# Optimization experiments

Measured on AMD Instinct MI355X. Metric: run time of the kernel, lower is better.

The kernel has to match this reference:

```python
import jax, jax.numpy as jnp
import numpy as np

B, N, D, H, KD, VD, O = 64, 2048, 256, 8, 32, 32, 256
LARGE = 1e9
EPS = 1e-10


def setup_inputs() -> dict:
    key = jax.random.key(0)
    ks = jax.random.split(key, 8)
    return {
        "q_data": jax.random.normal(ks[0], (B, N, D), dtype=jnp.float32),
        "m_data": jax.random.normal(ks[1], (B, N, D), dtype=jnp.float32),
        "q_mask": jnp.ones((B, N, 1), dtype=jnp.float32),
        "query_w": jax.random.normal(ks[2], (D, H, KD), dtype=jnp.float32) * 0.05,
        "key_w": jax.random.normal(ks[3], (D, KD), dtype=jnp.float32) * 0.05,
        "value_w": jax.random.normal(ks[4], (D, VD), dtype=jnp.float32) * 0.05,
        "gating_w": jax.random.normal(ks[5], (D, H, VD), dtype=jnp.float32) * 0.05,
        "gating_b": jnp.ones((H, VD), dtype=jnp.float32),
        "output_w": jax.random.normal(ks[6], (H, VD, O), dtype=jnp.float32) * 0.05,
        "output_b": jnp.zeros((O,), dtype=jnp.float32),
    }


def reference(q_data, m_data, q_mask, query_w, key_w, value_w, gating_w, gating_b, output_w, output_b):
    key_dim = query_w.shape[-1]
    # values/keys are shared across heads: [B, N, KD/VD]
    v = jnp.einsum('bka,ac->bkc', m_data, value_w)
    # masked mean over the query axis -> single query per batch element
    q_avg = jnp.sum(q_mask * q_data, axis=1) / (jnp.sum(q_mask, axis=1) + EPS)  # [B, D]
    q = jnp.einsum('ba,ahc->bhc', q_avg, query_w) * (key_dim ** -0.5)  # [B, H, KD]
    k = jnp.einsum('bka,ac->bkc', m_data, key_w)  # [B, N, KD]
    bias = LARGE * (q_mask[:, None, :, 0] - 1.0)  # [B, 1, N]
    logits = jnp.einsum('bhc,bkc->bhk', q, k) + bias  # [B, H, N]
    weights = jax.nn.softmax(logits, axis=-1)
    weighted_avg = jnp.einsum('bhk,bkc->bhc', weights, v)  # [B, H, VD]
    gate = jax.nn.sigmoid(jnp.einsum('bqc,chv->bqhv', q_data, gating_w) + gating_b)  # [B, N, H, VD]
    gated = weighted_avg[:, None] * gate  # broadcast single attn result over queries
    return jnp.einsum('bqhc,hco->bqo', gated, output_w) + output_b  # [B, N, O]
```

## Files before the change

kernel.cpp:

```cpp
#include <hip/hip_runtime.h>

#define B_ 64
#define N_ 2048
#define D_ 256
#define H_ 8
#define LARGE_ 1e9f
#define EPS_ 1e-10f

typedef __attribute__((ext_vector_type(4))) float f32x4;
typedef __attribute__((ext_vector_type(8))) short s16x8;

#define WS_QKBF 0
#define WS_WGP  524288
#define WS_QPART 655360
#define WS_MPART 1179648
#define WS_MX   1181696
#define WS_SM   1247232
#define WS_WA   1312768
#define WS_WMP  1378304
#define WS_WPP  1378304

__device__ __forceinline__ unsigned short f2bf(float f) {
  union { float f; unsigned u; } v; v.f = f;
  unsigned r = v.u + 0x7fffu + ((v.u >> 16) & 1u);
  return (unsigned short)(r >> 16);
}
__device__ __forceinline__ float bf2f(unsigned short s) {
  union { unsigned u; float f; } v; v.u = ((unsigned)s) << 16;
  return v.f;
}

__global__ void kA(const float* __restrict__ q_data, const float* __restrict__ q_mask,
                   const float* __restrict__ gating_w, float* __restrict__ qpart,
                   float* __restrict__ mpart, unsigned short* __restrict__ wgp) {
  int blk = blockIdx.x, t = threadIdx.x;
  if (blk < 512) {
    int b = blk >> 3, n0 = (blk & 7) * 256;
    __shared__ float msk[256];
    __shared__ float qred[4][256];
    __shared__ float mred[4];
    msk[t] = q_mask[b * N_ + n0 + t];
    __syncthreads();
    int w = t >> 6, d4 = t & 63;
    const float* qbase = q_data + ((size_t)(b * N_ + n0)) * D_;
    f32x4 acc = {0.f, 0.f, 0.f, 0.f};
    #pragma unroll 4
    for (int i = 0; i < 64; ++i) {
      int r = i * 4 + w;
      f32x4 v = *(const f32x4*)(qbase + (size_t)r * D_ + d4 * 4);
      float mk = msk[r];
      acc += v * mk;
    }
    *(f32x4*)(&qred[w][d4 * 4]) = acc;
    float mv = msk[t];
    for (int off = 32; off; off >>= 1) mv += __shfl_xor(mv, off);
    if ((t & 63) == 0) mred[t >> 6] = mv;
    __syncthreads();
    qpart[((size_t)blk) * 256 + t] = qred[0][t] + qred[1][t] + qred[2][t] + qred[3][t];
    if (t == 0) mpart[blk] = mred[0] + mred[1] + mred[2] + mred[3];
  } else {
    int base = (blk - 512) * 1024;
    for (int i = 0; i < 4; ++i) {
      int a = base + i * 256 + t;
      int sc = a >> 9, l = (a >> 3) & 63, j = a & 7;
      int s = sc >> 4, c = sc & 15, lh = l >> 4, ll = l & 15;
      int k = s * 32 + lh * 8 + j, n = c * 16 + ll;
      wgp[a] = f2bf(gating_w[k * 256 + n]);
    }
  }
}

__global__ void kB(const float* __restrict__ qpart, const float* __restrict__ mpart,
                   const float* __restrict__ query_w, const float* __restrict__ key_w,
                   unsigned short* __restrict__ qkbf) {
  int b = blockIdx.x, t = threadIdx.x;
  __shared__ float qa[256];
  __shared__ float ql[256];
  float s = 0.f;
  #pragma unroll
  for (int p = 0; p < 8; ++p) s += qpart[((size_t)(b * 8 + p)) * 256 + t];
  float ms = 0.f;
  #pragma unroll
  for (int p = 0; p < 8; ++p) ms += mpart[b * 8 + p];
  qa[t] = s / (ms + EPS_);
  __syncthreads();
  float acc = 0.f;
  #pragma unroll 4
  for (int a = 0; a < 256; ++a) acc += qa[a] * query_w[a * 256 + t];
  ql[t] = acc * 0.17677669529663687f;
  __syncthreads();
  float v8[8];
  #pragma unroll
  for (int h = 0; h < 8; ++h) {
    float v = 0.f;
    #pragma unroll
    for (int c = 0; c < 32; ++c) v += key_w[t * 32 + c] * ql[h * 32 + c];
    v8[h] = v;
  }
  int si = t >> 5, lh = (t >> 3) & 3, j = t & 7;
  unsigned short* base = qkbf + ((size_t)(b * 8 + si) * 64) * 8;
  #pragma unroll
  for (int h = 0; h < 8; ++h) {
    base[(lh * 16 + h) * 8 + j] = f2bf(v8[h]);
    base[(lh * 16 + 8 + h) * 8 + j] = 0;
  }
}

__global__ void kM(const float* __restrict__ m_data, const float* __restrict__ q_mask,
                   const unsigned short* __restrict__ qkbf, unsigned short* __restrict__ wm_part,
                   float* __restrict__ mx_part, float* __restrict__ sm_part) {
  int b = blockIdx.y, ch = blockIdx.x, n0 = ch * 64, t = threadIdx.x;
  __shared__ __align__(16) unsigned char sM[64 * 528];
  __shared__ f32x4 pW[64][2];
  __shared__ float red[4][8];
  __shared__ float hval[8];
  {
    int w = t >> 6, d4 = t & 63;
    #pragma unroll
    for (int i = 0; i < 16; ++i) {
      int r = i * 4 + w;
      f32x4 v = *(const f32x4*)(m_data + ((size_t)(b * N_ + n0 + r)) * D_ + d4 * 4);
      uint2 pp;
      pp.x = f2bf(v[0]) | ((unsigned)f2bf(v[1]) << 16);
      pp.y = f2bf(v[2]) | ((unsigned)f2bf(v[3]) << 16);
      *(uint2*)(sM + r * 528 + d4 * 8) = pp;
    }
  }
  __syncthreads();
  int lane = t & 63, w = t >> 6;
  int l15 = lane & 15, lhi = lane >> 4;
  const s16x8* A = (const s16x8*)qkbf + (size_t)b * 512;
  s16x8 areg[8];
  #pragma unroll
  for (int s = 0; s < 8; ++s) areg[s] = A[s * 64 + lane];
  f32x4 acc = {0.f, 0.f, 0.f, 0.f};
  int nrow = w * 16 + l15;
  #pragma unroll
  for (int s = 0; s < 8; ++s) {
    s16x8 bfr = *(const s16x8*)(sM + nrow * 528 + s * 64 + lhi * 16);
    acc = __builtin_amdgcn_mfma_f32_16x16x32_bf16(areg[s], bfr, acc, 0, 0, 0);
  }
  float bias = LARGE_ * (q_mask[b * N_ + n0 + nrow] - 1.f);
  float lg[4];
  #pragma unroll
  for (int r = 0; r < 4; ++r) lg[r] = (lhi < 2) ? (acc[r] + bias) : -3.4e38f;
  #pragma unroll
  for (int off = 8; off; off >>= 1)
    #pragma unroll
    for (int r = 0; r < 4; ++r) lg[r] = fmaxf(lg[r], __shfl_xor(lg[r], off));
  if (l15 == 0 && lhi < 2)
    #pragma unroll
    for (int r = 0; r < 4; ++r) red[w][lhi * 4 + r] = lg[r];
  __syncthreads();
  if (t < 8) {
    float m = fmaxf(fmaxf(red[0][t], red[1][t]), fmaxf(red[2][t], red[3][t]));
    hval[t] = m;
    mx_part[((size_t)(b * 32 + ch)) * 8 + t] = m;
  }
  __syncthreads();
  float pv[4], ps[4];
  #pragma unroll
  for (int r = 0; r < 4; ++r) {
    float M = hval[(lhi & 1) * 4 + r];
    float e = __expf(acc[r] + bias - M);
    pv[r] = e;
    ps[r] = (lhi < 2) ? e : 0.f;
  }
  if (lhi < 2) {
    f32x4 pq = {pv[0], pv[1], pv[2], pv[3]};
    pW[nrow][lhi] = pq;
  }
  #pragma unroll
  for (int off = 8; off; off >>= 1)
    #pragma unroll
    for (int r = 0; r < 4; ++r) ps[r] += __shfl_xor(ps[r], off);
  if (l15 == 0 && lhi < 2)
    #pragma unroll
    for (int r = 0; r < 4; ++r) red[w][lhi * 4 + r] = ps[r];
  __syncthreads();
  if (t < 8)
    sm_part[((size_t)(b * 32 + ch)) * 8 + t] = red[0][t] + red[1][t] + red[2][t] + red[3][t];
  f32x4 vacc[8];
  #pragma unroll
  for (int h = 0; h < 8; ++h) vacc[h] = (f32x4){0.f, 0.f, 0.f, 0.f};
  #pragma unroll 4
  for (int i = 0; i < 16; ++i) {
    int r = w * 16 + i;
    uint2 pp = *(const uint2*)(sM + r * 528 + lane * 8);
    f32x4 mv;
    mv[0] = bf2f(pp.x & 0xffff); mv[1] = bf2f(pp.x >> 16);
    mv[2] = bf2f(pp.y & 0xffff); mv[3] = bf2f(pp.y >> 16);
    f32x4 w0 = pW[r][0], w1 = pW[r][1];
    vacc[0] += mv * w0[0]; vacc[1] += mv * w0[1]; vacc[2] += mv * w0[2]; vacc[3] += mv * w0[3];
    vacc[4] += mv * w1[0]; vacc[5] += mv * w1[1]; vacc[6] += mv * w1[2]; vacc[7] += mv * w1[3];
  }
  __syncthreads();
  float* red2 = (float*)sM;
  #pragma unroll
  for (int h = 0; h < 8; ++h) *(f32x4*)(&red2[(w * 8 + h) * 256 + lane * 4]) = vacc[h];
  __syncthreads();
  float s8[8];
  #pragma unroll
  for (int h = 0; h < 8; ++h)
    s8[h] = red2[h * 256 + t] + red2[(8 + h) * 256 + t] + red2[(16 + h) * 256 + t] +
            red2[(24 + h) * 256 + t];
  uint4 u;
  u.x = f2bf(s8[0]) | ((unsigned)f2bf(s8[1]) << 16);
  u.y = f2bf(s8[2]) | ((unsigned)f2bf(s8[3]) << 16);
  u.z = f2bf(s8[4]) | ((unsigned)f2bf(s8[5]) << 16);
  u.w = f2bf(s8[6]) | ((unsigned)f2bf(s8[7]) << 16);
  *(uint4*)(wm_part + ((size_t)((b * 32 + ch) * 256 + t)) * 8) = u;
}

__global__ void kF1(const unsigned short* __restrict__ wm_part, const float* __restrict__ mx_part,
                    const float* __restrict__ sm_part, const float* __restrict__ value_w,
                    float* __restrict__ wa_g) {
  int b = blockIdx.x, t = threadIdx.x;
  __shared__ float s_mx[256], s_sm[256], scl[256];
  __shared__ float gmx[8], gden[8];
  __shared__ float wml[8][256];
  s_mx[t] = mx_part[(size_t)b * 256 + t];
  s_sm[t] = sm_part[(size_t)b * 256 + t];
  __syncthreads();
  if (t < 8) {
    float m = -3.4e38f;
    for (int c = 0; c < 32; ++c) m = fmaxf(m, s_mx[c * 8 + t]);
    gmx[t] = m;
  }
  __syncthreads();
  scl[t] = __expf(s_mx[t] - gmx[t & 7]);
  __syncthreads();
  if (t < 8) {
    float d = 0.f;
    for (int c = 0; c < 32; ++c) d += s_sm[c * 8 + t] * scl[c * 8 + t];
    gden[t] = d;
  }
  float acc[8] = {0.f, 0.f, 0.f, 0.f, 0.f, 0.f, 0.f, 0.f};
  for (int c = 0; c < 32; ++c) {
    uint4 u = *(const uint4*)(wm_part + ((size_t)((b * 32 + c) * 256 + t)) * 8);
    const float* sc = &scl[c * 8];
    acc[0] += bf2f(u.x & 0xffff) * sc[0]; acc[1] += bf2f(u.x >> 16) * sc[1];
    acc[2] += bf2f(u.y & 0xffff) * sc[2]; acc[3] += bf2f(u.y >> 16) * sc[3];
    acc[4] += bf2f(u.z & 0xffff) * sc[4]; acc[5] += bf2f(u.z >> 16) * sc[5];
    acc[6] += bf2f(u.w & 0xffff) * sc[6]; acc[7] += bf2f(u.w >> 16) * sc[7];
  }
  #pragma unroll
  for (int h = 0; h < 8; ++h) wml[h][t] = acc[h];
  __syncthreads();
  int h = t >> 5, v = t & 31;
  float s = 0.f;
  #pragma unroll 4
  for (int d = 0; d < 256; ++d) s += wml[h][d] * value_w[d * 32 + v];
  wa_g[b * 256 + t] = s / gden[h];
}

__global__ void kF2(const float* __restrict__ wa_g, const float* __restrict__ output_w,
                    unsigned short* __restrict__ wpp) {
  int blk = blockIdx.x, t = threadIdx.x;
  int b = blk >> 2, quad = blk & 3;
  __shared__ float wa[256];
  wa[t] = wa_g[b * 256 + t];
  __syncthreads();
  unsigned short* wp = wpp + (size_t)b * 65536;
  int base = quad * 16384;
  for (int it = 0; it < 64; ++it) {
    int a = base + it * 256 + t;
    int sc = a >> 9, l = (a >> 3) & 63, j = a & 7;
    int s = sc >> 4, c = sc & 15, lh = l >> 4, ll = l & 15;
    int hv = s * 32 + lh * 8 + j, o = c * 16 + ll;
    wp[a] = f2bf(wa[hv] * output_w[hv * 256 + o]);
  }
}

__global__ void __launch_bounds__(256, 4) kG(
    const float* __restrict__ q_data, const float* __restrict__ gating_b,
    const float* __restrict__ output_b, const unsigned short* __restrict__ wgp,
    const unsigned short* __restrict__ wpp, float* __restrict__ out) {
  int b = blockIdx.y, row0 = blockIdx.x * 64, t = threadIdx.x;
  __shared__ __align__(16) unsigned char sG[64 * 528];
  {
    int w = t >> 6, d4 = t & 63;
    #pragma unroll
    for (int i = 0; i < 16; ++i) {
      int r = i * 4 + w;
      f32x4 v = *(const f32x4*)(q_data + ((size_t)(b * N_ + row0 + r)) * D_ + d4 * 4);
      uint2 pp;
      pp.x = f2bf(v[0]) | ((unsigned)f2bf(v[1]) << 16);
      pp.y = f2bf(v[2]) | ((unsigned)f2bf(v[3]) << 16);
      *(uint2*)(sG + r * 528 + d4 * 8) = pp;
    }
  }
  __syncthreads();
  int lane = t & 63, cg = t >> 6;
  int l15 = lane & 15, lhi = lane >> 4;
  const f32x4 z = {0.f, 0.f, 0.f, 0.f};
  f32x4 acc[16];
  #pragma unroll
  for (int f = 0; f < 16; ++f) acc[f] = z;
  const s16x8* Bg = (const s16x8*)wgp;
  #pragma unroll
  for (int s = 0; s < 8; ++s) {
    s16x8 af[4], bfr[4];
    #pragma unroll
    for (int rt = 0; rt < 4; ++rt)
      af[rt] = *(const s16x8*)(sG + (rt * 16 + l15) * 528 + s * 64 + lhi * 16);
    #pragma unroll
    for (int ct = 0; ct < 4; ++ct) bfr[ct] = Bg[(s * 16 + cg * 4 + ct) * 64 + lane];
    #pragma unroll
    for (int rt = 0; rt < 4; ++rt)
      #pragma unroll
      for (int ct = 0; ct < 4; ++ct)
        acc[rt * 4 + ct] =
            __builtin_amdgcn_mfma_f32_16x16x32_bf16(af[rt], bfr[ct], acc[rt * 4 + ct], 0, 0, 0);
  }
  __syncthreads();
  {
    float gb[4];
    #pragma unroll
    for (int ct = 0; ct < 4; ++ct) gb[ct] = gating_b[cg * 64 + ct * 16 + l15];
    #pragma unroll
    for (int rt = 0; rt < 4; ++rt)
      #pragma unroll
      for (int ct = 0; ct < 4; ++ct) {
        int col = cg * 64 + ct * 16 + l15;
        #pragma unroll
        for (int r = 0; r < 4; ++r) {
          float x = acc[rt * 4 + ct][r] + gb[ct];
          float g = 1.f / (1.f + __expf(-x));
          int row = rt * 16 + lhi * 4 + r;
          *(unsigned short*)(sG + row * 528 + col * 2) = f2bf(g);
        }
      }
  }
  __syncthreads();
  #pragma unroll
  for (int f = 0; f < 16; ++f) acc[f] = z;
  const s16x8* Bp = (const s16x8*)wpp + (size_t)b * 8192;
  #pragma unroll
  for (int s = 0; s < 8; ++s) {
    s16x8 af[4], bfr[4];
    #pragma unroll
    for (int rt = 0; rt < 4; ++rt)
      af[rt] = *(const s16x8*)(sG + (rt * 16 + l15) * 528 + s * 64 + lhi * 16);
    #pragma unroll
    for (int ct = 0; ct < 4; ++ct) bfr[ct] = Bp[(s * 16 + cg * 4 + ct) * 64 + lane];
    #pragma unroll
    for (int rt = 0; rt < 4; ++rt)
      #pragma unroll
      for (int ct = 0; ct < 4; ++ct)
        acc[rt * 4 + ct] =
            __builtin_amdgcn_mfma_f32_16x16x32_bf16(af[rt], bfr[ct], acc[rt * 4 + ct], 0, 0, 0);
  }
  __syncthreads();
  float* fOut = (float*)sG;
  float ob[4];
  #pragma unroll
  for (int ct = 0; ct < 4; ++ct) ob[ct] = output_b[cg * 64 + ct * 16 + l15];
  #pragma unroll
  for (int p = 0; p < 2; ++p) {
    #pragma unroll
    for (int rt2 = 0; rt2 < 2; ++rt2) {
      int rt = p * 2 + rt2;
      #pragma unroll
      for (int ct = 0; ct < 4; ++ct) {
        int col = cg * 64 + ct * 16 + l15;
        #pragma unroll
        for (int r = 0; r < 4; ++r)
          fOut[(rt2 * 16 + lhi * 4 + r) * 260 + col] = acc[rt * 4 + ct][r] + ob[ct];
      }
    }
    __syncthreads();
    {
      int w = t >> 6, c4 = t & 63;
      #pragma unroll
      for (int j = 0; j < 8; ++j) {
        int r32 = j * 4 + w;
        f32x4 v = *(const f32x4*)(fOut + r32 * 260 + c4 * 4);
        *(f32x4*)(out + ((size_t)(b * N_ + row0 + p * 32 + r32)) * D_ + c4 * 4) = v;
      }
    }
    __syncthreads();
  }
}

extern "C" void kernel_launch(void* const* d_in, const int* in_sizes, int n_in,
                              void* d_out, int out_size, void* d_ws, size_t ws_size,
                              hipStream_t stream) {
  const float* q_data   = (const float*)d_in[0];
  const float* m_data   = (const float*)d_in[1];
  const float* q_mask   = (const float*)d_in[2];
  const float* query_w  = (const float*)d_in[3];
  const float* key_w    = (const float*)d_in[4];
  const float* value_w  = (const float*)d_in[5];
  const float* gating_w = (const float*)d_in[6];
  const float* gating_b = (const float*)d_in[7];
  const float* output_w = (const float*)d_in[8];
  const float* output_b = (const float*)d_in[9];
  float* out = (float*)d_out;
  char* ws = (char*)d_ws;

  unsigned short* qkbf = (unsigned short*)(ws + WS_QKBF);
  unsigned short* wgp  = (unsigned short*)(ws + WS_WGP);
  float* qpart = (float*)(ws + WS_QPART);
  float* mpart = (float*)(ws + WS_MPART);
  float* mx    = (float*)(ws + WS_MX);
  float* sm    = (float*)(ws + WS_SM);
  float* wa    = (float*)(ws + WS_WA);
  unsigned short* wmp = (unsigned short*)(ws + WS_WMP);
  unsigned short* wpp = (unsigned short*)(ws + WS_WPP);

  kA<<<576, 256, 0, stream>>>(q_data, q_mask, gating_w, qpart, mpart, wgp);
  kB<<<64, 256, 0, stream>>>(qpart, mpart, query_w, key_w, qkbf);
  kM<<<dim3(32, 64), 256, 0, stream>>>(m_data, q_mask, qkbf, wmp, mx, sm);
  kF1<<<64, 256, 0, stream>>>(wmp, mx, sm, value_w, wa);
  kF2<<<256, 256, 0, stream>>>(wa, output_w, wpp);
  kG<<<dim3(32, 64), 256, 0, stream>>>(q_data, gating_b, output_b, wgp, wpp, out);
}
```

Measured before the change: 478.4 us.

## Halve kG row tile for more blocks and stage output_w through LDS in kF2

The main gated-output kernel kG now handles 32 rows per block instead of 64. That doubles the grid, halves the accumulators and LDS per block, and raises the launch-bounds occupancy hint from 4 to 6. kF2 now copies output_w rows into shared memory with coalesced vector loads before doing the scattered, permuted bf16 packing, so it no longer makes strided global reads. The smaller kG tiles mean each weight fragment is reused across fewer rows, so wgp/wpp loads per output row roughly double.

```diff
diff --git a/kernel.cpp b/kernel.cpp
--- a/kernel.cpp
+++ b/kernel.cpp
@@ -258,30 +258,43 @@
                     unsigned short* __restrict__ wpp) {
   int blk = blockIdx.x, t = threadIdx.x;
   int b = blk >> 2, quad = blk & 3;
+  __shared__ float sOW[32 * 260];
   __shared__ float wa[256];
   wa[t] = wa_g[b * 256 + t];
-  __syncthreads();
   unsigned short* wp = wpp + (size_t)b * 65536;
-  int base = quad * 16384;
-  for (int it = 0; it < 64; ++it) {
-    int a = base + it * 256 + t;
-    int sc = a >> 9, l = (a >> 3) & 63, j = a & 7;
-    int s = sc >> 4, c = sc & 15, lh = l >> 4, ll = l & 15;
-    int hv = s * 32 + lh * 8 + j, o = c * 16 + ll;
-    wp[a] = f2bf(wa[hv] * output_w[hv * 256 + o]);
-  }
-}
-
-__global__ void __launch_bounds__(256, 4) kG(
+  for (int half = 0; half < 2; ++half) {
+    int srow = quad * 64 + half * 32;
+    __syncthreads();
+    const f32x4* src = (const f32x4*)(output_w + srow * 256);
+    #pragma unroll
+    for (int i = 0; i < 8; ++i) {
+      int idx4 = i * 256 + t;
+      f32x4 v = src[idx4];
+      int rr = idx4 >> 6, c4 = idx4 & 63;
+      *(f32x4*)(&sOW[rr * 260 + c4 * 4]) = v;
+    }
+    __syncthreads();
+    int abase = quad * 16384 + half * 8192;
+    for (int it = 0; it < 32; ++it) {
+      int a = abase + it * 256 + t;
+      int sc = a >> 9, l = (a >> 3) & 63, j = a & 7;
+      int c = sc & 15, lh = l >> 4, ll = l & 15;
+      int hvl = lh * 8 + j, o = c * 16 + ll;
+      wp[a] = f2bf(wa[srow + hvl] * sOW[hvl * 260 + o]);
+    }
+  }
+}
+
+__global__ void __launch_bounds__(256, 6) kG(
     const float* __restrict__ q_data, const float* __restrict__ gating_b,
     const float* __restrict__ output_b, const unsigned short* __restrict__ wgp,
     const unsigned short* __restrict__ wpp, float* __restrict__ out) {
-  int b = blockIdx.y, row0 = blockIdx.x * 64, t = threadIdx.x;
-  __shared__ __align__(16) unsigned char sG[64 * 528];
+  int b = blockIdx.y, row0 = blockIdx.x * 32, t = threadIdx.x;
+  __shared__ __align__(16) unsigned char sG[32 * 528];
   {
     int w = t >> 6, d4 = t & 63;
     #pragma unroll
-    for (int i = 0; i < 16; ++i) {
+    for (int i = 0; i < 8; ++i) {
       int r = i * 4 + w;
       f32x4 v = *(const f32x4*)(q_data + ((size_t)(b * N_ + row0 + r)) * D_ + d4 * 4);
       uint2 pp;
@@ -294,20 +307,20 @@
   int lane = t & 63, cg = t >> 6;
   int l15 = lane & 15, lhi = lane >> 4;
   const f32x4 z = {0.f, 0.f, 0.f, 0.f};
-  f32x4 acc[16];
-  #pragma unroll
-  for (int f = 0; f < 16; ++f) acc[f] = z;
+  f32x4 acc[8];
+  #pragma unroll
+  for (int f = 0; f < 8; ++f) acc[f] = z;
   const s16x8* Bg = (const s16x8*)wgp;
   #pragma unroll
   for (int s = 0; s < 8; ++s) {
-    s16x8 af[4], bfr[4];
-    #pragma unroll
-    for (int rt = 0; rt < 4; ++rt)
+    s16x8 af[2], bfr[4];
+    #pragma unroll
+    for (int rt = 0; rt < 2; ++rt)
       af[rt] = *(const s16x8*)(sG + (rt * 16 + l15) * 528 + s * 64 + lhi * 16);
     #pragma unroll
     for (int ct = 0; ct < 4; ++ct) bfr[ct] = Bg[(s * 16 + cg * 4 + ct) * 64 + lane];
     #pragma unroll
-    for (int rt = 0; rt < 4; ++rt)
+    for (int rt = 0; rt < 2; ++rt)
       #pragma unroll
       for (int ct = 0; ct < 4; ++ct)
         acc[rt * 4 + ct] =
@@ -319,7 +332,7 @@
     #pragma unroll
     for (int ct = 0; ct < 4; ++ct) gb[ct] = gating_b[cg * 64 + ct * 16 + l15];
     #pragma unroll
-    for (int rt = 0; rt < 4; ++rt)
+    for (int rt = 0; rt < 2; ++rt)
       #pragma unroll
       for (int ct = 0; ct < 4; ++ct) {
         int col = cg * 64 + ct * 16 + l15;
@@ -334,18 +347,18 @@
   }
   __syncthreads();
   #pragma unroll
-  for (int f = 0; f < 16; ++f) acc[f] = z;
+  for (int f = 0; f < 8; ++f) acc[f] = z;
   const s16x8* Bp = (const s16x8*)wpp + (size_t)b * 8192;
   #pragma unroll
   for (int s = 0; s < 8; ++s) {
-    s16x8 af[4], bfr[4];
-    #pragma unroll
-    for (int rt = 0; rt < 4; ++rt)
+    s16x8 af[2], bfr[4];
+    #pragma unroll
+    for (int rt = 0; rt < 2; ++rt)
       af[rt] = *(const s16x8*)(sG + (rt * 16 + l15) * 528 + s * 64 + lhi * 16);
     #pragma unroll
     for (int ct = 0; ct < 4; ++ct) bfr[ct] = Bp[(s * 16 + cg * 4 + ct) * 64 + lane];
     #pragma unroll
-    for (int rt = 0; rt < 4; ++rt)
+    for (int rt = 0; rt < 2; ++rt)
       #pragma unroll
       for (int ct = 0; ct < 4; ++ct)
         acc[rt * 4 + ct] =
@@ -359,24 +372,20 @@
   #pragma unroll
   for (int p = 0; p < 2; ++p) {
     #pragma unroll
-    for (int rt2 = 0; rt2 < 2; ++rt2) {
-      int rt = p * 2 + rt2;
+    for (int ct = 0; ct < 4; ++ct) {
+      int col = cg * 64 + ct * 16 + l15;
       #pragma unroll
-      for (int ct = 0; ct < 4; ++ct) {
-        int col = cg * 64 + ct * 16 + l15;
-        #pragma unroll
-        for (int r = 0; r < 4; ++r)
-          fOut[(rt2 * 16 + lhi * 4 + r) * 260 + col] = acc[rt * 4 + ct][r] + ob[ct];
-      }
+      for (int r = 0; r < 4; ++r)
+        fOut[(lhi * 4 + r) * 260 + col] = acc[p * 4 + ct][r] + ob[ct];
     }
     __syncthreads();
     {
       int w = t >> 6, c4 = t & 63;
       #pragma unroll
-      for (int j = 0; j < 8; ++j) {
-        int r32 = j * 4 + w;
-        f32x4 v = *(const f32x4*)(fOut + r32 * 260 + c4 * 4);
-        *(f32x4*)(out + ((size_t)(b * N_ + row0 + p * 32 + r32)) * D_ + c4 * 4) = v;
+      for (int j = 0; j < 4; ++j) {
+        int r16 = j * 4 + w;
+        f32x4 v = *(const f32x4*)(fOut + r16 * 260 + c4 * 4);
+        *(f32x4*)(out + ((size_t)(b * N_ + row0 + p * 16 + r16)) * D_ + c4 * 4) = v;
       }
     }
     __syncthreads();
@@ -414,5 +423,5 @@
   kM<<<dim3(32, 64), 256, 0, stream>>>(m_data, q_mask, qkbf, wmp, mx, sm);
   kF1<<<64, 256, 0, stream>>>(wmp, mx, sm, value_w, wa);
   kF2<<<256, 256, 0, stream>>>(wa, output_w, wpp);
-  kG<<<dim3(32, 64), 256, 0, stream>>>(q_data, gating_b, output_b, wgp, wpp, out);
-}
+  kG<<<dim3(64, 64), 256, 0, stream>>>(q_data, gating_b, output_b, wgp, wpp, out);
+}
```

Measured after the change: 502.9 us. 1.05x slower.
